# Kernel tuning notes

Measured on AMD Instinct MI355X. Metric: run time of the kernel, lower is better.

## Reference

```python
import jax, jax.numpy as jnp
import numpy as np

NUM_FREQS = 96
FRAME_SIZE = 5
LOOKAHEAD = 0


def setup_inputs() -> dict:
    key = jax.random.key(0)
    k1, k2 = jax.random.split(key)
    spec = jax.random.normal(k1, (32, 1, 1000, 481, 2), dtype=jnp.float32)
    coefs = 0.1 * jax.random.normal(k2, (32, 5, 1000, 96, 2), dtype=jnp.float32)
    return {"spec": spec, "coefs": coefs}


def reference(spec, coefs):
    # spec:  [B, 1, T, F, 2]  real/imag pairs
    # coefs: [B, O, T, F_df, 2], O = G * FRAME_SIZE (here G=1)
    B, C, T, F, _ = spec.shape
    fs = FRAME_SIZE
    spec_c = jax.lax.complex(spec[..., 0], spec[..., 1])        # [B,1,T,F]
    coefs_c = jax.lax.complex(coefs[..., 0], coefs[..., 1])     # [B,O,T,F_df]

    # Only the first NUM_FREQS bins are filtered; slice before windowing
    sp = spec_c[..., :NUM_FREQS]                                 # [B,1,T,F_df]
    if fs > 1:
        pad_l = fs - 1 - LOOKAHEAD
        sp = jnp.pad(sp, ((0, 0), (0, 0), (pad_l, LOOKAHEAD), (0, 0)))
        # sliding windows over time: [B,1,T,fs,F_df]
        idx = jnp.arange(T)[:, None] + jnp.arange(fs)[None, :]   # [T,fs]
        spec_f = sp[:, :, idx, :]                                # [B,1,T,fs,F_df]
    else:
        spec_f = sp[:, :, :, None, :]                            # [B,1,T,1,F_df]

    O = coefs_c.shape[1]
    cr = coefs_c.reshape(B, O // fs, fs, T, NUM_FREQS)           # [B,G,fs,T,F_df]
    # complex FIR per (t, f): sum over window taps n
    filt = jnp.einsum('bgtnf,bgntf->bgtf', spec_f, cr)           # [B,1,T,F_df]
    out_df = jnp.stack([filt.real, filt.imag], axis=-1)          # [B,1,T,F_df,2]
    return spec.at[..., :NUM_FREQS, :].set(out_df)
```

## Files before the change

### kernel.cpp

```cpp
#include <hip/hip_runtime.h>

constexpr int B  = 32;
constexpr int T  = 1000;
constexpr int F  = 481;
constexpr int NF = 96;
constexpr int FS = 5;

typedef float vf2 __attribute__((ext_vector_type(2)));
typedef float vf4 __attribute__((ext_vector_type(4)));

constexpr int FILTER_PAIRS   = B * T * (NF / 2);
constexpr int ROWS           = B * T;
constexpr int COPY_T_PER_ROW = 24;
constexpr int COPY_THREADS   = ROWS * COPY_T_PER_ROW;
constexpr int FILTER_BLOCKS  = FILTER_PAIRS / 256;
constexpr int COPY_BLOCKS    = COPY_THREADS / 256;
constexpr int TOTAL_BLOCKS   = FILTER_BLOCKS + COPY_BLOCKS;

__global__ void ldf_fused(const float* __restrict__ spec,
                          const float* __restrict__ coefs,
                          float* __restrict__ out) {
    const vf2* __restrict__ sp  = (const vf2*)spec;
    const vf4* __restrict__ sp4 = (const vf4*)spec;
    const vf4* __restrict__ cf4 = (const vf4*)coefs;
    vf2*       __restrict__ op  = (vf2*)out;
    vf4*       __restrict__ op4 = (vf4*)out;

    int bid = blockIdx.x;
    int k3  = bid / 3;
    int r3  = bid - k3 * 3;

    if (r3 < 2) {
        int fb  = 2 * k3 + r3;
        int gid = fb * 256 + threadIdx.x;

        int fp = gid % (NF / 2);
        int bt = gid / (NF / 2);
        int t  = bt % T;
        int b  = bt / T;
        int f0 = fp * 2;

        vf4  c[FS];
        vf2  s0[FS], s1[FS];
        float m[FS];
#pragma unroll
        for (int n = 0; n < FS; ++n) {
            int ts  = t + n - (FS - 1);
            int tsc = ts < 0 ? 0 : ts;
            m[n]    = ts < 0 ? 0.f : 1.f;
            c[n]    = cf4[((((b * FS + n) * T + t) * NF) + f0) >> 1];
            int sb  = (b * T + tsc) * F + f0;
            s0[n]   = sp[sb];
            s1[n]   = sp[sb + 1];
        }

        float re0 = 0.f, im0 = 0.f, re1 = 0.f, im1 = 0.f;
#pragma unroll
        for (int n = 0; n < FS; ++n) {
            float sx0 = s0[n].x * m[n], sy0 = s0[n].y * m[n];
            float sx1 = s1[n].x * m[n], sy1 = s1[n].y * m[n];
            re0 = fmaf(sx0, c[n].x, fmaf(-sy0, c[n].y, re0));
            im0 = fmaf(sx0, c[n].y, fmaf( sy0, c[n].x, im0));
            re1 = fmaf(sx1, c[n].z, fmaf(-sy1, c[n].w, re1));
            im1 = fmaf(sx1, c[n].w, fmaf( sy1, c[n].z, im1));
        }

        int o = (b * T + t) * F + f0;
        vf2 r0; r0.x = re0; r0.y = im0;
        vf2 r1; r1.x = re1; r1.y = im1;
        __builtin_nontemporal_store(r0, &op[o]);
        __builtin_nontemporal_store(r1, &op[o + 1]);
    } else {
        int cid = k3 * 256 + threadIdx.x;
        int rid = cid / COPY_T_PER_ROW;
        int k   = cid - rid * COPY_T_PER_ROW;
        int odd   = rid & 1;
        int basef = rid * (2 * F) + 192 + (odd << 1);
        int fbase = (basef >> 2) + k;

        vf4 v[8];
#pragma unroll
        for (int j = 0; j < 8; ++j) v[j] = sp4[fbase + COPY_T_PER_ROW * j];

        vf2 tv; int tidx = 0;
        if (k == 0) {
            int tf = rid * (2 * F) + (odd ? 192 : 960);
            tidx = tf >> 1;
            tv = sp[tidx];
        }
#pragma unroll
        for (int j = 0; j < 8; ++j)
            __builtin_nontemporal_store(v[j], &op4[fbase + COPY_T_PER_ROW * j]);
        if (k == 0)
            __builtin_nontemporal_store(tv, &op[tidx]);
    }
}

extern "C" void kernel_launch(void* const* d_in, const int* in_sizes, int n_in,
                              void* d_out, int out_size, void* d_ws, size_t ws_size,
                              hipStream_t stream) {
    const float* spec  = (const float*)d_in[0];
    const float* coefs = (const float*)d_in[1];
    float*       out   = (float*)d_out;

    ldf_fused<<<TOTAL_BLOCKS, 256, 0, stream>>>(spec, coefs, out);
}
```

Baseline: 66.57 us.

## Restructure kernel to one block per row with filter and copy lanes

Replaces the interleaved filter/copy block scheme with one 256-thread block per (b,t) row. Threads 0-47 compute the filtered bins, 48-239 copy the passthrough bins, and thread 240 copies the tail element. Block indices are swizzled across eight row groups, even rows use vf4 stores, and passthrough copies use nontemporal loads. This cuts the index division overhead and keeps each row's reads and writes in one block, at the cost of 15 idle threads per block and 32000 small blocks.

```diff
diff --git a/kernel.cpp b/kernel.cpp
--- a/kernel.cpp
+++ b/kernel.cpp
@@ -5,21 +5,14 @@
 constexpr int F  = 481;
 constexpr int NF = 96;
 constexpr int FS = 5;
+constexpr int ROWS = B * T;
 
 typedef float vf2 __attribute__((ext_vector_type(2)));
 typedef float vf4 __attribute__((ext_vector_type(4)));
 
-constexpr int FILTER_PAIRS   = B * T * (NF / 2);
-constexpr int ROWS           = B * T;
-constexpr int COPY_T_PER_ROW = 24;
-constexpr int COPY_THREADS   = ROWS * COPY_T_PER_ROW;
-constexpr int FILTER_BLOCKS  = FILTER_PAIRS / 256;
-constexpr int COPY_BLOCKS    = COPY_THREADS / 256;
-constexpr int TOTAL_BLOCKS   = FILTER_BLOCKS + COPY_BLOCKS;
-
-__global__ void ldf_fused(const float* __restrict__ spec,
-                          const float* __restrict__ coefs,
-                          float* __restrict__ out) {
+__global__ __launch_bounds__(256) void ldf_row(const float* __restrict__ spec,
+                                               const float* __restrict__ coefs,
+                                               float* __restrict__ out) {
     const vf2* __restrict__ sp  = (const vf2*)spec;
     const vf4* __restrict__ sp4 = (const vf4*)spec;
     const vf4* __restrict__ cf4 = (const vf4*)coefs;
@@ -27,19 +20,15 @@
     vf4*       __restrict__ op4 = (vf4*)out;
 
     int bid = blockIdx.x;
-    int k3  = bid / 3;
-    int r3  = bid - k3 * 3;
+    int rid = (bid & 7) * (ROWS / 8) + (bid >> 3);
+    int b   = rid / T;
+    int t   = rid - b * T;
+    int rowf = rid * (2 * F);
+    int odd  = rid & 1;
+    int tid  = threadIdx.x;
 
-    if (r3 < 2) {
-        int fb  = 2 * k3 + r3;
-        int gid = fb * 256 + threadIdx.x;
-
-        int fp = gid % (NF / 2);
-        int bt = gid / (NF / 2);
-        int t  = bt % T;
-        int b  = bt / T;
-        int f0 = fp * 2;
-
+    if (tid < 48) {
+        int k = tid;
         vf4  c[FS];
         vf2  s0[FS], s1[FS];
         float m[FS];
@@ -48,12 +37,11 @@
             int ts  = t + n - (FS - 1);
             int tsc = ts < 0 ? 0 : ts;
             m[n]    = ts < 0 ? 0.f : 1.f;
-            c[n]    = cf4[((((b * FS + n) * T + t) * NF) + f0) >> 1];
-            int sb  = (b * T + tsc) * F + f0;
+            c[n]    = cf4[((b * FS + n) * T + t) * (NF / 2) + k];
+            int sb  = (b * T + tsc) * F + 2 * k;
             s0[n]   = sp[sb];
             s1[n]   = sp[sb + 1];
         }
-
         float re0 = 0.f, im0 = 0.f, re1 = 0.f, im1 = 0.f;
 #pragma unroll
         for (int n = 0; n < FS; ++n) {
@@ -64,35 +52,24 @@
             re1 = fmaf(sx1, c[n].z, fmaf(-sy1, c[n].w, re1));
             im1 = fmaf(sx1, c[n].w, fmaf( sy1, c[n].z, im1));
         }
-
-        int o = (b * T + t) * F + f0;
-        vf2 r0; r0.x = re0; r0.y = im0;
-        vf2 r1; r1.x = re1; r1.y = im1;
-        __builtin_nontemporal_store(r0, &op[o]);
-        __builtin_nontemporal_store(r1, &op[o + 1]);
-    } else {
-        int cid = k3 * 256 + threadIdx.x;
-        int rid = cid / COPY_T_PER_ROW;
-        int k   = cid - rid * COPY_T_PER_ROW;
-        int odd   = rid & 1;
-        int basef = rid * (2 * F) + 192 + (odd << 1);
-        int fbase = (basef >> 2) + k;
-
-        vf4 v[8];
-#pragma unroll
-        for (int j = 0; j < 8; ++j) v[j] = sp4[fbase + COPY_T_PER_ROW * j];
-
-        vf2 tv; int tidx = 0;
-        if (k == 0) {
-            int tf = rid * (2 * F) + (odd ? 192 : 960);
-            tidx = tf >> 1;
-            tv = sp[tidx];
+        if (!odd) {
+            vf4 r; r.x = re0; r.y = im0; r.z = re1; r.w = im1;
+            __builtin_nontemporal_store(r, &op4[rowf / 4 + k]);
+        } else {
+            vf2 r0; r0.x = re0; r0.y = im0;
+            vf2 r1; r1.x = re1; r1.y = im1;
+            __builtin_nontemporal_store(r0, &op[rowf / 2 + 2 * k]);
+            __builtin_nontemporal_store(r1, &op[rowf / 2 + 2 * k + 1]);
         }
-#pragma unroll
-        for (int j = 0; j < 8; ++j)
-            __builtin_nontemporal_store(v[j], &op4[fbase + COPY_T_PER_ROW * j]);
-        if (k == 0)
-            __builtin_nontemporal_store(tv, &op[tidx]);
+    } else if (tid < 240) {
+        int k2    = tid - 48;
+        int basef = rowf + 192 + 2 * odd;
+        vf4 v = __builtin_nontemporal_load(&sp4[basef / 4 + k2]);
+        __builtin_nontemporal_store(v, &op4[basef / 4 + k2]);
+    } else if (tid == 240) {
+        int tf = rowf + (odd ? 192 : 960);
+        vf2 v = __builtin_nontemporal_load(&sp[tf / 2]);
+        __builtin_nontemporal_store(v, &op[tf / 2]);
     }
 }
 
@@ -103,5 +80,5 @@
     const float* coefs = (const float*)d_in[1];
     float*       out   = (float*)d_out;
 
-    ldf_fused<<<TOTAL_BLOCKS, 256, 0, stream>>>(spec, coefs, out);
+    ldf_row<<<ROWS, 256, 0, stream>>>(spec, coefs, out);
 }
```

Result: faster. 58.85 us (-11.6%).
